# Optimization experiments

Hardware: AMD Instinct MI355X
Metric: run time of the kernel (lower is better)

Reference implementation:

```python
import jax, jax.numpy as jnp
import numpy as np

H = 4          # heads (both HGTConv and MHA)
LN_EPS = 1e-5
ALPHA = 0.1


def _ln(x, g, b):
    m = x.mean(-1, keepdims=True)
    v = ((x - m) ** 2).mean(-1, keepdims=True)
    return (x - m) * jax.lax.rsqrt(v + LN_EPS) * g + b


def _kqv(x, Wk, bk, Wq, bq, Wv, bv, D):
    N = x.shape[0]
    k = (x @ Wk.T + bk).reshape(N, H, D)
    q = (x @ Wq.T + bq).reshape(N, H, D)
    v = (x @ Wv.T + bv).reshape(N, H, D)
    return k, q, v


def _hgt_edge(q_dst, k_src, v_src, a_rel, m_rel, p_rel, src, dst, n_dst):
    """PyG HGTConv message passing for one edge type: relation-transform,
    per-dst-node softmax, weighted scatter-sum."""
    D = q_dst.shape[-1]
    k = jnp.einsum('nhd,hde->nhe', k_src, a_rel)   # [N_src,H,D]
    v = jnp.einsum('nhd,hde->nhe', v_src, m_rel)
    logit = (q_dst[dst] * k[src]).sum(-1) * p_rel / np.sqrt(D)   # [E,H]
    mx = jax.ops.segment_max(logit, dst, num_segments=n_dst)
    e = jnp.exp(logit - mx[dst])
    s = jax.ops.segment_sum(e, dst, num_segments=n_dst)
    a = e / (s[dst] + 1e-16)
    return jax.ops.segment_sum(v[src] * a[..., None], dst, num_segments=n_dst)  # [N_dst,H,D]


def _hgt_out(agg, x, Wout, bout, skip):
    N, dim = x.shape
    o = jax.nn.gelu(agg.reshape(N, dim), approximate=False) @ Wout.T + bout
    a = jax.nn.sigmoid(skip)
    return a * o + (1.0 - a) * x


def _mha(x, Wi, bi, Wo, bo):
    # self-attention over all entities as a single sequence (batch=1)
    N, dim = x.shape
    D = dim // H
    q, k, v = jnp.split(x @ Wi.T + bi, 3, axis=-1)
    q = q.reshape(N, H, D).transpose(1, 0, 2)
    k = k.reshape(N, H, D).transpose(1, 0, 2)
    v = v.reshape(N, H, D).transpose(1, 0, 2)
    att = jax.nn.softmax(jnp.einsum('hnd,hmd->hnm', q, k) / np.sqrt(D), axis=-1)
    o = jnp.einsum('hnm,hmd->hnd', att, v).transpose(1, 0, 2).reshape(N, dim)
    return o @ Wo.T + bo


def _forward(x_entity, x_passage, query_emb,
             Wk_ent, bk_ent, Wq_ent, bq_ent, Wv_ent, bv_ent, Wout_ent, bout_ent, skip_ent,
             Wk_psg, bk_psg, Wq_psg, bq_psg, Wv_psg, bv_psg, Wout_psg, bout_psg, skip_psg,
             a_e2p, m_e2p, p_e2p, a_p2e, m_p2e, p_p2e,
             mha_in_w, mha_in_b, mha_out_w, mha_out_b,
             ln_ent_g, ln_ent_b, ln_psg_g, ln_psg_b,
             w1, b1, w2, b2,
             e2p_src, e2p_dst, p2e_src, p2e_dst):
    N_e, dim = x_entity.shape
    N_p = x_passage.shape[0]
    D = dim // H
    # ---- HGTConv ----
    k_e, q_e, v_e = _kqv(x_entity, Wk_ent, bk_ent, Wq_ent, bq_ent, Wv_ent, bv_ent, D)
    k_p, q_p, v_p = _kqv(x_passage, Wk_psg, bk_psg, Wq_psg, bq_psg, Wv_psg, bv_psg, D)
    agg_p = _hgt_edge(q_p, k_e, v_e, a_e2p, m_e2p, p_e2p, e2p_src, e2p_dst, N_p)
    agg_e = _hgt_edge(q_e, k_p, v_p, a_p2e, m_p2e, p_p2e, p2e_src, p2e_dst, N_e)
    h_ent = _hgt_out(agg_e, x_entity, Wout_ent, bout_ent, skip_ent)
    h_psg = _hgt_out(agg_p, x_passage, Wout_psg, bout_psg, skip_psg)
    # ---- global entity attention + residual mix + LN ----
    h_glob = _mha(h_ent, mha_in_w, mha_in_b, mha_out_w, mha_out_b)
    h_ent = _ln((1.0 - ALPHA) * h_ent + ALPHA * h_glob, ln_ent_g, ln_ent_b)
    # ---- gather-scale-scatter entity -> passage (kernel target) ----
    q = query_emb.reshape(-1)
    rel = jax.nn.sigmoid(h_ent @ q)                          # [N_e]
    w_ent = h_ent[e2p_src] * rel[e2p_src][:, None]           # gather + scale
    ctx = jax.ops.segment_sum(w_ent, e2p_dst, num_segments=N_p)  # scatter-add
    h_psg = _ln(h_psg + ctx, ln_psg_g, ln_psg_b)
    # ---- scoring head ----
    feats = jnp.concatenate([h_psg, jnp.broadcast_to(q, (N_p, dim))], axis=-1)
    scores = (jax.nn.relu(feats @ w1.T + b1) @ w2.T + b2).squeeze(-1)
    return scores


def setup_inputs() -> dict:
    key = jax.random.key(0)
    N_E, N_P, DIM, NE = 4096, 4096, 256, 262144
    D = DIM // H
    ks = iter(jax.random.split(key, 64))
    def rn(shape, s=1.0):
        return jax.random.normal(next(ks), shape, jnp.float32) * s
    w = 0.05
    inp = {
        'x_entity': rn((N_E, DIM)),
        'x_passage': rn((N_P, DIM)),
        'query_emb': rn((DIM,)),
    }
    for t in ('ent', 'psg'):
        inp['Wk_' + t] = rn((DIM, DIM), w); inp['bk_' + t] = jnp.zeros((DIM,))
        inp['Wq_' + t] = rn((DIM, DIM), w); inp['bq_' + t] = jnp.zeros((DIM,))
        inp['Wv_' + t] = rn((DIM, DIM), w); inp['bv_' + t] = jnp.zeros((DIM,))
        inp['Wout_' + t] = rn((DIM, DIM), w); inp['bout_' + t] = jnp.zeros((DIM,))
        inp['skip_' + t] = jnp.ones(())
    for e in ('e2p', 'p2e'):
        inp['a_' + e] = rn((H, D, D), w)
        inp['m_' + e] = rn((H, D, D), w)
        inp['p_' + e] = jnp.ones((H,))
    inp['mha_in_w'] = rn((3 * DIM, DIM), w); inp['mha_in_b'] = jnp.zeros((3 * DIM,))
    inp['mha_out_w'] = rn((DIM, DIM), w); inp['mha_out_b'] = jnp.zeros((DIM,))
    inp['ln_ent_g'] = jnp.ones((DIM,)); inp['ln_ent_b'] = jnp.zeros((DIM,))
    inp['ln_psg_g'] = jnp.ones((DIM,)); inp['ln_psg_b'] = jnp.zeros((DIM,))
    inp['w1'] = rn((DIM, 2 * DIM), w); inp['b1'] = jnp.zeros((DIM,))
    inp['w2'] = rn((1, DIM), w); inp['b2'] = jnp.zeros((1,))
    inp['e2p_src'] = jax.random.randint(next(ks), (NE,), 0, N_E, jnp.int32)
    inp['e2p_dst'] = jax.random.randint(next(ks), (NE,), 0, N_P, jnp.int32)
    inp['p2e_src'] = jax.random.randint(next(ks), (NE,), 0, N_P, jnp.int32)
    inp['p2e_dst'] = jax.random.randint(next(ks), (NE,), 0, N_E, jnp.int32)
    return inp


def reference(x_entity, x_passage, query_emb,
              Wk_ent, bk_ent, Wq_ent, bq_ent, Wv_ent, bv_ent, Wout_ent, bout_ent, skip_ent,
              Wk_psg, bk_psg, Wq_psg, bq_psg, Wv_psg, bv_psg, Wout_psg, bout_psg, skip_psg,
              a_e2p, m_e2p, p_e2p, a_p2e, m_p2e, p_p2e,
              mha_in_w, mha_in_b, mha_out_w, mha_out_b,
              ln_ent_g, ln_ent_b, ln_psg_g, ln_psg_b,
              w1, b1, w2, b2,
              e2p_src, e2p_dst, p2e_src, p2e_dst):
    return _forward(x_entity, x_passage, query_emb,
                    Wk_ent, bk_ent, Wq_ent, bq_ent, Wv_ent, bv_ent, Wout_ent, bout_ent, skip_ent,
                    Wk_psg, bk_psg, Wq_psg, bq_psg, Wv_psg, bv_psg, Wout_psg, bout_psg, skip_psg,
                    a_e2p, m_e2p, p_e2p, a_p2e, m_p2e, p_p2e,
                    mha_in_w, mha_in_b, mha_out_w, mha_out_b,
                    ln_ent_g, ln_ent_b, ln_psg_g, ln_psg_b,
                    w1, b1, w2, b2,
                    e2p_src, e2p_dst, p2e_src, p2e_dst)
```

## Files before the change

### kernel.cpp

```cpp
#include <hip/hip_runtime.h>
#include <hip/hip_bf16.h>
#include <math.h>

#define DIM 256
#define NHEAD 4
#define HD 64
#define MSPLIT 4

typedef __attribute__((ext_vector_type(8))) short short8b;
typedef __attribute__((ext_vector_type(4))) float f32x4;

union B8 { uint4 u; short8b v; };

__device__ __forceinline__ float sigmoidf_(float x) { return 1.0f / (1.0f + __expf(-x)); }
__device__ __forceinline__ float geluf_(float x) {
    return 0.5f * x * (1.0f + erff(x * 0.70710678118654752440f));
}
__device__ __forceinline__ float wave_sum64(float v) {
    v += __shfl_xor(v, 32); v += __shfl_xor(v, 16); v += __shfl_xor(v, 8);
    v += __shfl_xor(v, 4);  v += __shfl_xor(v, 2);  v += __shfl_xor(v, 1);
    return v;
}
__device__ __forceinline__ unsigned short f2bf(float f) {
    union { float f; unsigned int u; } a; a.f = f;
    unsigned int u = a.u;
    unsigned int r = (u + 0x7FFFu + ((u >> 16) & 1u)) >> 16;
    return (unsigned short)r;
}
__device__ __forceinline__ unsigned int pk2bf(float lo, float hi) {
    return (unsigned int)f2bf(lo) | ((unsigned int)f2bf(hi) << 16);
}

template<int IN_GELU, int OUT_MODE, int WBF>
__launch_bounds__(256)
__global__ void gemm_kernel(const float* __restrict__ A, int lda,
                            const float* __restrict__ W0, const float* __restrict__ W1,
                            const float* __restrict__ W2, int ldw,
                            const float* __restrict__ B0, const float* __restrict__ B1,
                            const float* __restrict__ B2,
                            float* __restrict__ C, int ldc, int Kin,
                            const float* __restrict__ xres,
                            const float* __restrict__ skipv,
                            float* __restrict__ scores,
                            const float* __restrict__ w2v,
                            const float* __restrict__ b2v,
                            unsigned short* __restrict__ Cbf)
{
    __shared__ float As[16][68];
    __shared__ float Ws[16][68];
    const int t = threadIdx.x;
    const int r0 = blockIdx.y * 64;
    const int c0 = blockIdx.x * 64;
    const int widx = c0 >> 8;
    const float* W  = (widx == 0) ? W0 : (widx == 1 ? W1 : W2);
    const float* Bv = (widx == 0) ? B0 : (widx == 1 ? B1 : B2);
    const int cw = c0 & 255;

    const int lrow = t >> 2;
    const int lk   = (t & 3) << 2;
    const int ty = t >> 4, tx = t & 15;

    const float* Aptr = A + (size_t)(r0 + lrow) * lda + lk;
    const float* Wptr = W + (size_t)(cw + lrow) * ldw + lk;

    float acc[4][4] = {};
    for (int k0 = 0; k0 < Kin; k0 += 16) {
        float4 av = *reinterpret_cast<const float4*>(Aptr + k0);
        float4 wv = *reinterpret_cast<const float4*>(Wptr + k0);
        if (IN_GELU) {
            av.x = geluf_(av.x); av.y = geluf_(av.y);
            av.z = geluf_(av.z); av.w = geluf_(av.w);
        }
        As[lk + 0][lrow] = av.x; As[lk + 1][lrow] = av.y;
        As[lk + 2][lrow] = av.z; As[lk + 3][lrow] = av.w;
        Ws[lk + 0][lrow] = wv.x; Ws[lk + 1][lrow] = wv.y;
        Ws[lk + 2][lrow] = wv.z; Ws[lk + 3][lrow] = wv.w;
        __syncthreads();
#pragma unroll
        for (int k = 0; k < 16; ++k) {
            const float4 a = *reinterpret_cast<const float4*>(&As[k][ty << 2]);
            const float4 b = *reinterpret_cast<const float4*>(&Ws[k][tx << 2]);
            const float ar[4] = {a.x, a.y, a.z, a.w};
            const float br[4] = {b.x, b.y, b.z, b.w};
#pragma unroll
            for (int i = 0; i < 4; ++i)
#pragma unroll
                for (int j = 0; j < 4; ++j)
                    acc[i][j] = fmaf(ar[i], br[j], acc[i][j]);
        }
        __syncthreads();
    }

    float bias[4];
#pragma unroll
    for (int j = 0; j < 4; ++j) bias[j] = Bv[cw + (tx << 2) + j];

    if (OUT_MODE == 0) {
#pragma unroll
        for (int i = 0; i < 4; ++i) {
            const int r = r0 + (ty << 2) + i;
            float4 st;
            st.x = acc[i][0] + bias[0]; st.y = acc[i][1] + bias[1];
            st.z = acc[i][2] + bias[2]; st.w = acc[i][3] + bias[3];
            *reinterpret_cast<float4*>(&C[(size_t)r * ldc + c0 + (tx << 2)]) = st;
            if (WBF) {
                ushort4 sb;
                sb.x = f2bf(st.x); sb.y = f2bf(st.y); sb.z = f2bf(st.z); sb.w = f2bf(st.w);
                *reinterpret_cast<ushort4*>(&Cbf[(size_t)r * ldc + c0 + (tx << 2)]) = sb;
            }
        }
    } else if (OUT_MODE == 1) {
        const float sg = sigmoidf_(skipv[0]);
#pragma unroll
        for (int i = 0; i < 4; ++i) {
            const int r = r0 + (ty << 2) + i;
            const float4 xv = *reinterpret_cast<const float4*>(&xres[(size_t)r * ldc + c0 + (tx << 2)]);
            float4 st;
            st.x = sg * (acc[i][0] + bias[0]) + (1.f - sg) * xv.x;
            st.y = sg * (acc[i][1] + bias[1]) + (1.f - sg) * xv.y;
            st.z = sg * (acc[i][2] + bias[2]) + (1.f - sg) * xv.z;
            st.w = sg * (acc[i][3] + bias[3]) + (1.f - sg) * xv.w;
            *reinterpret_cast<float4*>(&C[(size_t)r * ldc + c0 + (tx << 2)]) = st;
        }
    } else {
        float wv[4];
#pragma unroll
        for (int j = 0; j < 4; ++j) wv[j] = w2v[c0 + (tx << 2) + j];
#pragma unroll
        for (int i = 0; i < 4; ++i) {
            float p = 0.f;
#pragma unroll
            for (int j = 0; j < 4; ++j)
                p = fmaf(fmaxf(acc[i][j] + bias[j], 0.f), wv[j], p);
            if (c0 == 0 && tx == 0) p += b2v[0];
            atomicAdd(&scores[r0 + (ty << 2) + i], p);
        }
    }
}

__launch_bounds__(256)
__global__ void rel_transform_kernel(const float* __restrict__ kin, int ldin,
                                     const float* __restrict__ arel,
                                     float* __restrict__ kout)
{
    __shared__ float Al[64][68];
    __shared__ float Kl[64][65];
    const int t = threadIdx.x;
    const int r0 = blockIdx.x * 64;
    const int h = blockIdx.y;
    const float* ah = arel + h * 4096;
    for (int i = t; i < 1024; i += 256) {
        const int rr = i >> 4, c4 = (i & 15) << 2;
        const float4 av = *reinterpret_cast<const float4*>(&ah[rr * 64 + c4]);
        *reinterpret_cast<float4*>(&Al[rr][c4]) = av;
        const float4 kv = *reinterpret_cast<const float4*>(&kin[(size_t)(r0 + rr) * ldin + h * 64 + c4]);
        Kl[rr][c4 + 0] = kv.x; Kl[rr][c4 + 1] = kv.y;
        Kl[rr][c4 + 2] = kv.z; Kl[rr][c4 + 3] = kv.w;
    }
    __syncthreads();
    const int r  = t & 63;
    const int e0 = (t >> 6) << 4;
    float acc[16] = {};
    for (int d = 0; d < 64; ++d) {
        const float kv = Kl[r][d];
#pragma unroll
        for (int u4 = 0; u4 < 4; ++u4) {
            const float4 a = *reinterpret_cast<const float4*>(&Al[d][e0 + (u4 << 2)]);
            acc[u4 * 4 + 0] = fmaf(kv, a.x, acc[u4 * 4 + 0]);
            acc[u4 * 4 + 1] = fmaf(kv, a.y, acc[u4 * 4 + 1]);
            acc[u4 * 4 + 2] = fmaf(kv, a.z, acc[u4 * 4 + 2]);
            acc[u4 * 4 + 3] = fmaf(kv, a.w, acc[u4 * 4 + 3]);
        }
    }
#pragma unroll
    for (int u4 = 0; u4 < 4; ++u4) {
        float4 st = {acc[u4 * 4 + 0], acc[u4 * 4 + 1], acc[u4 * 4 + 2], acc[u4 * 4 + 3]};
        *reinterpret_cast<float4*>(&kout[(size_t)(r0 + r) * 256 + h * 64 + e0 + (u4 << 2)]) = st;
    }
}

__global__ void edge_count_kernel(const int* __restrict__ dst, int* __restrict__ cnt, int E)
{
    const int i = blockIdx.x * 256 + threadIdx.x;
    if (i < E) atomicAdd(&cnt[dst[i]], 1);
}

__launch_bounds__(1024)
__global__ void scan_kernel(const int* __restrict__ cnt, int* __restrict__ indptr,
                            int* __restrict__ cursor)
{
    __shared__ int sh[1024];
    const int t = threadIdx.x;
    const int4 v = *reinterpret_cast<const int4*>(&cnt[t << 2]);
    const int sum = v.x + v.y + v.z + v.w;
    sh[t] = sum;
    __syncthreads();
    for (int off = 1; off < 1024; off <<= 1) {
        int x = 0;
        if (t >= off) x = sh[t - off];
        __syncthreads();
        if (t >= off) sh[t] += x;
        __syncthreads();
    }
    int run = sh[t] - sum;
    const int base = t << 2;
    if (t == 0) indptr[0] = 0;
    cursor[base + 0] = run; run += v.x; indptr[base + 1] = run;
    cursor[base + 1] = run; run += v.y; indptr[base + 2] = run;
    cursor[base + 2] = run; run += v.z; indptr[base + 3] = run;
    cursor[base + 3] = run; run += v.w; indptr[base + 4] = run;
}

__global__ void edge_scatter_kernel(const int* __restrict__ src, const int* __restrict__ dst,
                                    int* __restrict__ cursor, int* __restrict__ ssrc, int E)
{
    const int i = blockIdx.x * 256 + threadIdx.x;
    if (i < E) {
        const int p = atomicAdd(&cursor[dst[i]], 1);
        ssrc[p] = src[i];
    }
}

__launch_bounds__(256)
__global__ void hgt_attn_kernel(const float* __restrict__ qdst,
                                const float* __restrict__ kt,
                                const float* __restrict__ vt,
                                const float* __restrict__ prel,
                                const int* __restrict__ indptr,
                                const int* __restrict__ ssrc,
                                float* __restrict__ agg)
{
    const int n = blockIdx.x * 4 + (threadIdx.x >> 6);
    const int lane = threadIdx.x & 63;
    const int h = lane >> 4;
    const int d4 = (lane & 15) << 2;
    const float4 q = *reinterpret_cast<const float4*>(&qdst[(size_t)n * 768 + h * 64 + d4]);
    const float ps = prel[h] * 0.125f;
    const int e0 = indptr[n], e1 = indptr[n + 1];
    float m = -1e30f, s = 0.f;
    float4 acc = {0.f, 0.f, 0.f, 0.f};
    for (int e = e0; e < e1; ++e) {
        const int sr = ssrc[e];
        const float4 k = *reinterpret_cast<const float4*>(&kt[(size_t)sr * 256 + h * 64 + d4]);
        float d = q.x * k.x + q.y * k.y + q.z * k.z + q.w * k.w;
        d += __shfl_xor(d, 1); d += __shfl_xor(d, 2);
        d += __shfl_xor(d, 4); d += __shfl_xor(d, 8);
        const float logit = d * ps;
        const float mn = fmaxf(m, logit);
        const float f = __expf(m - mn);
        const float p = __expf(logit - mn);
        s = s * f + p;
        const float4 v = *reinterpret_cast<const float4*>(&vt[(size_t)sr * 256 + h * 64 + d4]);
        acc.x = acc.x * f + p * v.x;
        acc.y = acc.y * f + p * v.y;
        acc.z = acc.z * f + p * v.z;
        acc.w = acc.w * f + p * v.w;
        m = mn;
    }
    const float inv = 1.f / (s + 1e-16f);
    float4 st = {acc.x * inv, acc.y * inv, acc.z * inv, acc.w * inv};
    *reinterpret_cast<float4*>(&agg[(size_t)n * 256 + h * 64 + d4]) = st;
}

__launch_bounds__(256)
__global__ void vtrans_kernel(const unsigned short* __restrict__ qkv_bf,
                              unsigned short* __restrict__ vt, int N)
{
    __shared__ unsigned short tile[64][66];
    const int t = threadIdx.x;
    const int k0 = blockIdx.x * 64;
    const int h = blockIdx.y;
    {
        const int key = t >> 2;
        const int d0 = (t & 3) << 4;
        const unsigned short* src = qkv_bf + (size_t)(k0 + key) * 768 + 512 + h * 64 + d0;
        const uint4 a = *reinterpret_cast<const uint4*>(src);
        const uint4 b = *reinterpret_cast<const uint4*>(src + 8);
        const unsigned int w_[8] = {a.x, a.y, a.z, a.w, b.x, b.y, b.z, b.w};
#pragma unroll
        for (int j = 0; j < 8; ++j) {
            tile[d0 + 2 * j][key]     = (unsigned short)(w_[j] & 0xffff);
            tile[d0 + 2 * j + 1][key] = (unsigned short)(w_[j] >> 16);
        }
    }
    __syncthreads();
    {
        const int d = t >> 2;
        const int kk = (t & 3) << 4;
        unsigned int o_[8];
#pragma unroll
        for (int j = 0; j < 8; ++j)
            o_[j] = (unsigned int)tile[d][kk + 2 * j] | ((unsigned int)tile[d][kk + 2 * j + 1] << 16);
        unsigned short* dstp = vt + (size_t)(h * 64 + d) * N + k0 + kk;
        uint4 s0 = {o_[0], o_[1], o_[2], o_[3]};
        uint4 s1 = {o_[4], o_[5], o_[6], o_[7]};
        *reinterpret_cast<uint4*>(dstp) = s0;
        *reinterpret_cast<uint4*>(dstp + 8) = s1;
    }
}

__launch_bounds__(256)
__global__ void mha_mfma_kernel(const unsigned short* __restrict__ qkv_bf,
                                const unsigned short* __restrict__ vt_bf,
                                float* __restrict__ opart,
                                float* __restrict__ mpart,
                                float* __restrict__ lpart,
                                int N)
{
    const int lane = threadIdx.x & 63;
    const int g = lane >> 4;
    const int q15 = lane & 15;
    const int gw = blockIdx.x * 4 + (threadIdx.x >> 6);
    const int split = gw & (MSPLIT - 1);
    const int gq = gw >> 2;
    const int h = gq >> 8;
    const int qt = gq & 255;
    const int q0 = qt * 16;
    const int kbeg = split * (N / MSPLIT);
    const int kend = kbeg + (N / MSPLIT);

    B8 qf0, qf1;
    {
        const unsigned short* qp = qkv_bf + (size_t)(q0 + q15) * 768 + h * 64 + g * 8;
        qf0.u = *reinterpret_cast<const uint4*>(qp);
        qf1.u = *reinterpret_cast<const uint4*>(qp + 32);
    }

    f32x4 o0 = {0,0,0,0}, o1 = {0,0,0,0}, o2 = {0,0,0,0}, o3 = {0,0,0,0};
    float m_run = -1e30f, l_run = 0.f;

    const unsigned short* kbase = qkv_bf + 256 + h * 64 + g * 8;
    const unsigned short* vbase = vt_bf + (size_t)(h * 64 + q15) * N + g * 8;
    const int sl0 = (((2 * g) & 3) << 4) + q15;
    const int sl1 = (((2 * g + 1) & 3) << 4) + q15;

    for (int ck = kbeg; ck < kend; ck += 32) {
        B8 k00, k01, k10, k11;
        const unsigned short* kp0 = kbase + (size_t)(ck + q15) * 768;
        const unsigned short* kp1 = kbase + (size_t)(ck + 16 + q15) * 768;
        k00.u = *reinterpret_cast<const uint4*>(kp0);
        k01.u = *reinterpret_cast<const uint4*>(kp0 + 32);
        k10.u = *reinterpret_cast<const uint4*>(kp1);
        k11.u = *reinterpret_cast<const uint4*>(kp1 + 32);
        f32x4 s0 = {0,0,0,0}, s1 = {0,0,0,0};
        s0 = __builtin_amdgcn_mfma_f32_16x16x32_bf16(k00.v, qf0.v, s0, 0, 0, 0);
        s0 = __builtin_amdgcn_mfma_f32_16x16x32_bf16(k01.v, qf1.v, s0, 0, 0, 0);
        s1 = __builtin_amdgcn_mfma_f32_16x16x32_bf16(k10.v, qf0.v, s1, 0, 0, 0);
        s1 = __builtin_amdgcn_mfma_f32_16x16x32_bf16(k11.v, qf1.v, s1, 0, 0, 0);

        float p[8];
        p[0] = s0.x * 0.125f; p[1] = s0.y * 0.125f; p[2] = s0.z * 0.125f; p[3] = s0.w * 0.125f;
        p[4] = s1.x * 0.125f; p[5] = s1.y * 0.125f; p[6] = s1.z * 0.125f; p[7] = s1.w * 0.125f;

        float mx = fmaxf(fmaxf(fmaxf(p[0], p[1]), fmaxf(p[2], p[3])),
                         fmaxf(fmaxf(p[4], p[5]), fmaxf(p[6], p[7])));
        mx = fmaxf(mx, __shfl_xor(mx, 16));
        mx = fmaxf(mx, __shfl_xor(mx, 32));
        const float mnew = fmaxf(m_run, mx);
        const float f = __expf(m_run - mnew);
        float sum = 0.f;
#pragma unroll
        for (int i = 0; i < 8; ++i) { p[i] = __expf(p[i] - mnew); sum += p[i]; }
        sum += __shfl_xor(sum, 16);
        sum += __shfl_xor(sum, 32);
        l_run = l_run * f + sum;
        m_run = mnew;
        o0 *= f; o1 *= f; o2 *= f; o3 *= f;

        const unsigned int c01a = pk2bf(p[0], p[1]), c23a = pk2bf(p[2], p[3]);
        const unsigned int c01b = pk2bf(p[4], p[5]), c23b = pk2bf(p[6], p[7]);
        uint4 pu;
        {
            unsigned int x0, x1;
            x0 = (unsigned int)__shfl((int)c01a, sl0); x1 = (unsigned int)__shfl((int)c01b, sl0);
            pu.x = (g < 2) ? x0 : x1;
            x0 = (unsigned int)__shfl((int)c23a, sl0); x1 = (unsigned int)__shfl((int)c23b, sl0);
            pu.y = (g < 2) ? x0 : x1;
            x0 = (unsigned int)__shfl((int)c01a, sl1); x1 = (unsigned int)__shfl((int)c01b, sl1);
            pu.z = (g < 2) ? x0 : x1;
            x0 = (unsigned int)__shfl((int)c23a, sl1); x1 = (unsigned int)__shfl((int)c23b, sl1);
            pu.w = (g < 2) ? x0 : x1;
        }
        B8 pb; pb.u = pu;

        const unsigned short* vp = vbase + ck;
        B8 vf;
        vf.u = *reinterpret_cast<const uint4*>(vp);
        o0 = __builtin_amdgcn_mfma_f32_16x16x32_bf16(vf.v, pb.v, o0, 0, 0, 0);
        vf.u = *reinterpret_cast<const uint4*>(vp + (size_t)16 * N);
        o1 = __builtin_amdgcn_mfma_f32_16x16x32_bf16(vf.v, pb.v, o1, 0, 0, 0);
        vf.u = *reinterpret_cast<const uint4*>(vp + (size_t)32 * N);
        o2 = __builtin_amdgcn_mfma_f32_16x16x32_bf16(vf.v, pb.v, o2, 0, 0, 0);
        vf.u = *reinterpret_cast<const uint4*>(vp + (size_t)48 * N);
        o3 = __builtin_amdgcn_mfma_f32_16x16x32_bf16(vf.v, pb.v, o3, 0, 0, 0);
    }

    float* op = opart + (size_t)split * N * 256 + (size_t)(q0 + q15) * 256 + h * 64 + 4 * g;
#pragma unroll
    for (int r = 0; r < 4; ++r) {
        op[0 * 16 + r] = o0[r];
        op[1 * 16 + r] = o1[r];
        op[2 * 16 + r] = o2[r];
        op[3 * 16 + r] = o3[r];
    }
    if (g == 0) {
        mpart[(size_t)(split * NHEAD + h) * N + q0 + q15] = m_run;
        lpart[(size_t)(split * NHEAD + h) * N + q0 + q15] = l_run;
    }
}

__launch_bounds__(256)
__global__ void mha_combine_kernel(const float* __restrict__ opart,
                                   const float* __restrict__ mpart,
                                   const float* __restrict__ lpart,
                                   float* __restrict__ outp, int N)
{
    const int q = blockIdx.x;
    const int c = threadIdx.x;
    const int h = c >> 6;
    const size_t base = (size_t)q * 256 + c;
    float m[MSPLIT], l[MSPLIT];
    float M = -1e30f;
#pragma unroll
    for (int s = 0; s < MSPLIT; ++s) {
        m[s] = mpart[(size_t)(s * NHEAD + h) * N + q];
        l[s] = lpart[(size_t)(s * NHEAD + h) * N + q];
        M = fmaxf(M, m[s]);
    }
    float L = 0.f, o = 0.f;
#pragma unroll
    for (int s = 0; s < MSPLIT; ++s) {
        const float w = __expf(m[s] - M);
        L += w * l[s];
        o = fmaf(w, opart[(size_t)s * N * 256 + base], o);
    }
    outp[base] = o / L;
}

__launch_bounds__(256)
__global__ void mix_ln_rel_kernel(float* __restrict__ he, const float* __restrict__ hg,
                                  const float* __restrict__ g, const float* __restrict__ b,
                                  const float* __restrict__ q, float* __restrict__ rel)
{
    const int row = (blockIdx.x * 256 + threadIdx.x) >> 6;
    const int lane = threadIdx.x & 63;
    const float4 a = *reinterpret_cast<const float4*>(&he[(size_t)row * 256 + (lane << 2)]);
    const float4 c = *reinterpret_cast<const float4*>(&hg[(size_t)row * 256 + (lane << 2)]);
    float4 v;
    v.x = 0.9f * a.x + 0.1f * c.x; v.y = 0.9f * a.y + 0.1f * c.y;
    v.z = 0.9f * a.z + 0.1f * c.z; v.w = 0.9f * a.w + 0.1f * c.w;
    const float mean = wave_sum64(v.x + v.y + v.z + v.w) * (1.f / 256.f);
    float4 d = {v.x - mean, v.y - mean, v.z - mean, v.w - mean};
    const float var = wave_sum64(d.x * d.x + d.y * d.y + d.z * d.z + d.w * d.w) * (1.f / 256.f);
    const float rs = rsqrtf(var + 1e-5f);
    const float4 gg = *reinterpret_cast<const float4*>(&g[lane << 2]);
    const float4 bb = *reinterpret_cast<const float4*>(&b[lane << 2]);
    float4 y = {d.x * rs * gg.x + bb.x, d.y * rs * gg.y + bb.y,
                d.z * rs * gg.z + bb.z, d.w * rs * gg.w + bb.w};
    *reinterpret_cast<float4*>(&he[(size_t)row * 256 + (lane << 2)]) = y;
    const float4 qq = *reinterpret_cast<const float4*>(&q[lane << 2]);
    const float dq = wave_sum64(y.x * qq.x + y.y * qq.y + y.z * qq.z + y.w * qq.w);
    if (lane == 0) rel[row] = sigmoidf_(dq);
}

__launch_bounds__(256)
__global__ void ctx_gather_kernel(const float* __restrict__ he, const float* __restrict__ rel,
                                  const int* __restrict__ indptr, const int* __restrict__ ssrc,
                                  float* __restrict__ ctx)
{
    const int gw = (blockIdx.x * 256 + threadIdx.x) >> 6;
    const int lane = threadIdx.x & 63;
    const int p = gw >> 2, qt = gw & 3;
    const int e0 = indptr[p], e1 = indptr[p + 1];
    float acc = 0.f;
    for (int e = e0; e < e1; ++e) {
        const int sr = ssrc[e];
        acc = fmaf(he[(size_t)sr * 256 + qt * 64 + lane], rel[sr], acc);
    }
    ctx[(size_t)p * 256 + qt * 64 + lane] = acc;
}

__launch_bounds__(256)
__global__ void psg_ln_kernel(float* __restrict__ hp, const float* __restrict__ ctx,
                              const float* __restrict__ g, const float* __restrict__ b)
{
    const int row = (blockIdx.x * 256 + threadIdx.x) >> 6;
    const int lane = threadIdx.x & 63;
    const float4 a = *reinterpret_cast<const float4*>(&hp[(size_t)row * 256 + (lane << 2)]);
    const float4 c = *reinterpret_cast<const float4*>(&ctx[(size_t)row * 256 + (lane << 2)]);
    float4 v = {a.x + c.x, a.y + c.y, a.z + c.z, a.w + c.w};
    const float mean = wave_sum64(v.x + v.y + v.z + v.w) * (1.f / 256.f);
    float4 d = {v.x - mean, v.y - mean, v.z - mean, v.w - mean};
    const float var = wave_sum64(d.x * d.x + d.y * d.y + d.z * d.z + d.w * d.w) * (1.f / 256.f);
    const float rs = rsqrtf(var + 1e-5f);
    const float4 gg = *reinterpret_cast<const float4*>(&g[lane << 2]);
    const float4 bb = *reinterpret_cast<const float4*>(&b[lane << 2]);
    float4 y = {d.x * rs * gg.x + bb.x, d.y * rs * gg.y + bb.y,
                d.z * rs * gg.z + bb.z, d.w * rs * gg.w + bb.w};
    *reinterpret_cast<float4*>(&hp[(size_t)row * 256 + (lane << 2)]) = y;
}

__global__ void qterm_kernel(const float* __restrict__ w1, const float* __restrict__ b1,
                             const float* __restrict__ q, float* __restrict__ qterm)
{
    __shared__ float qs[256];
    const int t = threadIdx.x;
    qs[t] = q[t];
    __syncthreads();
    float s = b1[t];
    for (int k = 0; k < 256; ++k) s = fmaf(w1[(size_t)t * 512 + 256 + k], qs[k], s);
    qterm[t] = s;
}

extern "C" void kernel_launch(void* const* d_in, const int* in_sizes, int n_in,
                              void* d_out, int out_size, void* d_ws, size_t ws_size,
                              hipStream_t stream)
{
    const float* x_ent = (const float*)d_in[0];
    const float* x_psg = (const float*)d_in[1];
    const float* q_emb = (const float*)d_in[2];
    const float* Wk_e = (const float*)d_in[3];  const float* bk_e = (const float*)d_in[4];
    const float* Wq_e = (const float*)d_in[5];  const float* bq_e = (const float*)d_in[6];
    const float* Wv_e = (const float*)d_in[7];  const float* bv_e = (const float*)d_in[8];
    const float* Wo_e = (const float*)d_in[9];  const float* bo_e = (const float*)d_in[10];
    const float* sk_e = (const float*)d_in[11];
    const float* Wk_p = (const float*)d_in[12]; const float* bk_p = (const float*)d_in[13];
    const float* Wq_p = (const float*)d_in[14]; const float* bq_p = (const float*)d_in[15];
    const float* Wv_p = (const float*)d_in[16]; const float* bv_p = (const float*)d_in[17];
    const float* Wo_p = (const float*)d_in[18]; const float* bo_p = (const float*)d_in[19];
    const float* sk_p = (const float*)d_in[20];
    const float* a_e2p = (const float*)d_in[21];
    const float* m_e2p = (const float*)d_in[22];
    const float* p_e2p = (const float*)d_in[23];
    const float* a_p2e = (const float*)d_in[24];
    const float* m_p2e = (const float*)d_in[25];
    const float* p_p2e = (const float*)d_in[26];
    const float* Wmi = (const float*)d_in[27];  const float* bmi = (const float*)d_in[28];
    const float* Wmo = (const float*)d_in[29];  const float* bmo = (const float*)d_in[30];
    const float* lng_e = (const float*)d_in[31]; const float* lnb_e = (const float*)d_in[32];
    const float* lng_p = (const float*)d_in[33]; const float* lnb_p = (const float*)d_in[34];
    const float* w1 = (const float*)d_in[35];   const float* b1 = (const float*)d_in[36];
    const float* w2 = (const float*)d_in[37];   const float* b2 = (const float*)d_in[38];
    const int* e2p_src = (const int*)d_in[39];
    const int* e2p_dst = (const int*)d_in[40];
    const int* p2e_src = (const int*)d_in[41];
    const int* p2e_dst = (const int*)d_in[42];

    const int NE = in_sizes[0] / DIM;
    const int NP = in_sizes[1] / DIM;
    const int E  = in_sizes[39];
    float* scores = (float*)d_out;

    char* wp = (char*)d_ws;
    auto alloc = [&](size_t bytes) -> void* {
        void* r = (void*)wp;
        wp += (bytes + 255) & ~(size_t)255;
        return r;
    };
    float* kqv_e = (float*)alloc((size_t)NE * 768 * 4);
    float* kqv_p = (float*)alloc((size_t)NP * 768 * 4);
    float* kt_e  = (float*)alloc((size_t)NE * 256 * 4);
    float* vt_e  = (float*)alloc((size_t)NE * 256 * 4);
    float* kt_p  = (float*)alloc((size_t)NP * 256 * 4);
    float* vt_p  = (float*)alloc((size_t)NP * 256 * 4);
    float* agg_p = (float*)alloc((size_t)NP * 256 * 4);
    float* agg_e = (float*)alloc((size_t)NE * 256 * 4);
    float* h_ent = (float*)alloc((size_t)NE * 256 * 4);
    float* h_psg = (float*)alloc((size_t)NP * 256 * 4);
    float* qkv_m = (float*)alloc((size_t)NE * 768 * 4);
    float* att_o = (float*)alloc((size_t)NE * 256 * 4);
    float* h_glob= (float*)alloc((size_t)NE * 256 * 4);
    float* relv  = (float*)alloc((size_t)NE * 4);
    float* ctxb  = (float*)alloc((size_t)NP * 256 * 4);
    float* qterm = (float*)alloc(256 * 4);
    unsigned short* qkv_bf = (unsigned short*)alloc((size_t)NE * 768 * 2);
    unsigned short* vt_bf  = (unsigned short*)alloc((size_t)256 * NE * 2);
    float* mpart = (float*)alloc((size_t)MSPLIT * NHEAD * NE * 4);
    float* lpart = (float*)alloc((size_t)MSPLIT * NHEAD * NE * 4);
    float* opart = kqv_e;
    int* cnt_a = (int*)alloc((size_t)NP * 4);
    int* cur_a = (int*)alloc((size_t)NP * 4);
    int* ip_a  = (int*)alloc((size_t)(NP + 1) * 4);
    int* ss_a  = (int*)alloc((size_t)E * 4);
    int* cnt_b = (int*)alloc((size_t)NE * 4);
    int* cur_b = (int*)alloc((size_t)NE * 4);
    int* ip_b  = (int*)alloc((size_t)(NE + 1) * 4);
    int* ss_b  = (int*)alloc((size_t)E * 4);

    hipMemsetAsync(cnt_a, 0, (size_t)NP * 4, stream);
    hipMemsetAsync(cnt_b, 0, (size_t)NE * 4, stream);
    hipMemsetAsync(d_out, 0, (size_t)out_size * 4, stream);

    const int eb = (E + 255) / 256;
    edge_count_kernel<<<eb, 256, 0, stream>>>(e2p_dst, cnt_a, E);
    edge_count_kernel<<<eb, 256, 0, stream>>>(p2e_dst, cnt_b, E);
    scan_kernel<<<1, 1024, 0, stream>>>(cnt_a, ip_a, cur_a);
    scan_kernel<<<1, 1024, 0, stream>>>(cnt_b, ip_b, cur_b);
    edge_scatter_kernel<<<eb, 256, 0, stream>>>(e2p_src, e2p_dst, cur_a, ss_a, E);
    edge_scatter_kernel<<<eb, 256, 0, stream>>>(p2e_src, p2e_dst, cur_b, ss_b, E);

    gemm_kernel<0,0,0><<<dim3(12, NE / 64), 256, 0, stream>>>(
        x_ent, 256, Wk_e, Wq_e, Wv_e, 256, bk_e, bq_e, bv_e,
        kqv_e, 768, 256, nullptr, nullptr, nullptr, nullptr, nullptr, nullptr);
    gemm_kernel<0,0,0><<<dim3(12, NP / 64), 256, 0, stream>>>(
        x_psg, 256, Wk_p, Wq_p, Wv_p, 256, bk_p, bq_p, bv_p,
        kqv_p, 768, 256, nullptr, nullptr, nullptr, nullptr, nullptr, nullptr);

    rel_transform_kernel<<<dim3(NE / 64, NHEAD), 256, 0, stream>>>(kqv_e + 0,   768, a_e2p, kt_e);
    rel_transform_kernel<<<dim3(NE / 64, NHEAD), 256, 0, stream>>>(kqv_e + 512, 768, m_e2p, vt_e);
    rel_transform_kernel<<<dim3(NP / 64, NHEAD), 256, 0, stream>>>(kqv_p + 0,   768, a_p2e, kt_p);
    rel_transform_kernel<<<dim3(NP / 64, NHEAD), 256, 0, stream>>>(kqv_p + 512, 768, m_p2e, vt_p);

    hgt_attn_kernel<<<NP / 4, 256, 0, stream>>>(kqv_p + 256, kt_e, vt_e, p_e2p, ip_a, ss_a, agg_p);
    hgt_attn_kernel<<<NE / 4, 256, 0, stream>>>(kqv_e + 256, kt_p, vt_p, p_p2e, ip_b, ss_b, agg_e);

    gemm_kernel<1,1,0><<<dim3(4, NE / 64), 256, 0, stream>>>(
        agg_e, 256, Wo_e, Wo_e, Wo_e, 256, bo_e, bo_e, bo_e,
        h_ent, 256, 256, x_ent, sk_e, nullptr, nullptr, nullptr, nullptr);
    gemm_kernel<1,1,0><<<dim3(4, NP / 64), 256, 0, stream>>>(
        agg_p, 256, Wo_p, Wo_p, Wo_p, 256, bo_p, bo_p, bo_p,
        h_psg, 256, 256, x_psg, sk_p, nullptr, nullptr, nullptr, nullptr);

    gemm_kernel<0,0,1><<<dim3(12, NE / 64), 256, 0, stream>>>(
        h_ent, 256, Wmi, Wmi + 65536, Wmi + 131072, 256, bmi, bmi + 256, bmi + 512,
        qkv_m, 768, 256, nullptr, nullptr, nullptr, nullptr, nullptr, qkv_bf);
    vtrans_kernel<<<dim3(NE / 64, NHEAD), 256, 0, stream>>>(qkv_bf, vt_bf, NE);
    mha_mfma_kernel<<<NHEAD * (NE / 16) * MSPLIT / 4, 256, 0, stream>>>(
        qkv_bf, vt_bf, opart, mpart, lpart, NE);
    mha_combine_kernel<<<NE, 256, 0, stream>>>(opart, mpart, lpart, att_o, NE);
    gemm_kernel<0,0,0><<<dim3(4, NE / 64), 256, 0, stream>>>(
        att_o, 256, Wmo, Wmo, Wmo, 256, bmo, bmo, bmo,
        h_glob, 256, 256, nullptr, nullptr, nullptr, nullptr, nullptr, nullptr);

    mix_ln_rel_kernel<<<NE / 4, 256, 0, stream>>>(h_ent, h_glob, lng_e, lnb_e, q_emb, relv);

    ctx_gather_kernel<<<NP, 256, 0, stream>>>(h_ent, relv, ip_a, ss_a, ctxb);
    psg_ln_kernel<<<NP / 4, 256, 0, stream>>>(h_psg, ctxb, lng_p, lnb_p);

    qterm_kernel<<<1, 256, 0, stream>>>(w1, b1, q_emb, qterm);
    gemm_kernel<0,2,0><<<dim3(4, NP / 64), 256, 0, stream>>>(
        h_psg, 256, w1, w1, w1, 512, qterm, qterm, qterm,
        nullptr, 256, 256, nullptr, nullptr, scores, w2, b2, nullptr);
}
```

Baseline: 758.6 us.

## Move dense projection GEMMs to bf16 MFMA with pre-converted weights and activations

Adds kernels that convert the twelve 256x256 weight matrices and the input or GELU'd activations to bf16. It then replaces the fp32 FMA tiled GEMMs for the KQV, output, MHA-in and MHA-out projections with a bf16 MFMA kernel that reads operands straight from global memory. The MHA combine now writes bf16 so the out-projection can read it directly, and the MHA-in GEMM writes only bf16. This moves the GEMMs onto the matrix cores at the cost of extra conversion launches, reduced precision, uncoalesced scalar epilogue stores and no LDS reuse.

```diff
diff --git a/kernel.cpp b/kernel.cpp
--- a/kernel.cpp
+++ b/kernel.cpp
@@ -31,7 +31,121 @@
     return (unsigned int)f2bf(lo) | ((unsigned int)f2bf(hi) << 16);
 }
 
-template<int IN_GELU, int OUT_MODE, int WBF>
+template<int DO_GELU>
+__launch_bounds__(256)
+__global__ void cvt_bf16_kernel(const float* __restrict__ src,
+                                unsigned short* __restrict__ dst, int n8)
+{
+    const int i = blockIdx.x * 256 + threadIdx.x;
+    if (i >= n8) return;
+    float4 a = reinterpret_cast<const float4*>(src)[2 * i];
+    float4 b = reinterpret_cast<const float4*>(src)[2 * i + 1];
+    if (DO_GELU) {
+        a.x = geluf_(a.x); a.y = geluf_(a.y); a.z = geluf_(a.z); a.w = geluf_(a.w);
+        b.x = geluf_(b.x); b.y = geluf_(b.y); b.z = geluf_(b.z); b.w = geluf_(b.w);
+    }
+    ushort4 lo = {f2bf(a.x), f2bf(a.y), f2bf(a.z), f2bf(a.w)};
+    ushort4 hi = {f2bf(b.x), f2bf(b.y), f2bf(b.z), f2bf(b.w)};
+    reinterpret_cast<ushort4*>(dst)[2 * i] = lo;
+    reinterpret_cast<ushort4*>(dst)[2 * i + 1] = hi;
+}
+
+__launch_bounds__(256)
+__global__ void cvt_w_kernel(const float* __restrict__ W0, const float* __restrict__ W1,
+                             const float* __restrict__ W2, const float* __restrict__ W3,
+                             const float* __restrict__ W4, const float* __restrict__ W5,
+                             const float* __restrict__ W6, const float* __restrict__ W7,
+                             const float* __restrict__ W8, const float* __restrict__ W9,
+                             const float* __restrict__ W10, const float* __restrict__ W11,
+                             unsigned short* __restrict__ arena)
+{
+    const float* s;
+    switch (blockIdx.y) {
+        case 0: s = W0; break;  case 1: s = W1; break;  case 2: s = W2; break;
+        case 3: s = W3; break;  case 4: s = W4; break;  case 5: s = W5; break;
+        case 6: s = W6; break;  case 7: s = W7; break;  case 8: s = W8; break;
+        case 9: s = W9; break;  case 10: s = W10; break; default: s = W11; break;
+    }
+    const int i = blockIdx.x * 256 + threadIdx.x;
+    unsigned short* dst = arena + (size_t)blockIdx.y * 65536;
+    float4 a = reinterpret_cast<const float4*>(s)[2 * i];
+    float4 b = reinterpret_cast<const float4*>(s)[2 * i + 1];
+    ushort4 lo = {f2bf(a.x), f2bf(a.y), f2bf(a.z), f2bf(a.w)};
+    ushort4 hi = {f2bf(b.x), f2bf(b.y), f2bf(b.z), f2bf(b.w)};
+    reinterpret_cast<ushort4*>(dst)[2 * i] = lo;
+    reinterpret_cast<ushort4*>(dst)[2 * i + 1] = hi;
+}
+
+template<int OUT_MODE, int WF32, int WBF>
+__launch_bounds__(256)
+__global__ void bgemm_kernel(const unsigned short* __restrict__ Abf,
+                             const unsigned short* __restrict__ W0b,
+                             const unsigned short* __restrict__ W1b,
+                             const unsigned short* __restrict__ W2b,
+                             const float* __restrict__ B0, const float* __restrict__ B1,
+                             const float* __restrict__ B2,
+                             float* __restrict__ C, int ldc,
+                             unsigned short* __restrict__ Cbf, int ldcb,
+                             const float* __restrict__ xres,
+                             const float* __restrict__ skipv)
+{
+    const int t = threadIdx.x;
+    const int lane = t & 63;
+    const int wid = t >> 6;
+    const int col16 = lane & 15;
+    const int oct = lane >> 4;
+    const int r0 = blockIdx.y * 64 + wid * 16;
+    const int c0 = blockIdx.x * 64;
+    const int widx = c0 >> 8;
+    const unsigned short* W = (widx == 0) ? W0b : (widx == 1 ? W1b : W2b);
+    const float* Bv = (widx == 0) ? B0 : (widx == 1 ? B1 : B2);
+    const int cw = c0 & 255;
+
+    const unsigned short* aptr = Abf + (size_t)(r0 + col16) * 256 + oct * 8;
+    const unsigned short* wptr = W + (size_t)(cw + col16) * 256 + oct * 8;
+
+    f32x4 acc0 = {0,0,0,0}, acc1 = {0,0,0,0}, acc2 = {0,0,0,0}, acc3 = {0,0,0,0};
+#pragma unroll
+    for (int k0 = 0; k0 < 256; k0 += 32) {
+        B8 af, w0, w1, w2, w3;
+        af.u = *reinterpret_cast<const uint4*>(aptr + k0);
+        w0.u = *reinterpret_cast<const uint4*>(wptr + k0);
+        w1.u = *reinterpret_cast<const uint4*>(wptr + k0 + 16 * 256);
+        w2.u = *reinterpret_cast<const uint4*>(wptr + k0 + 32 * 256);
+        w3.u = *reinterpret_cast<const uint4*>(wptr + k0 + 48 * 256);
+        acc0 = __builtin_amdgcn_mfma_f32_16x16x32_bf16(af.v, w0.v, acc0, 0, 0, 0);
+        acc1 = __builtin_amdgcn_mfma_f32_16x16x32_bf16(af.v, w1.v, acc1, 0, 0, 0);
+        acc2 = __builtin_amdgcn_mfma_f32_16x16x32_bf16(af.v, w2.v, acc2, 0, 0, 0);
+        acc3 = __builtin_amdgcn_mfma_f32_16x16x32_bf16(af.v, w3.v, acc3, 0, 0, 0);
+    }
+
+    float bias[4];
+#pragma unroll
+    for (int j = 0; j < 4; ++j) bias[j] = Bv[cw + j * 16 + col16];
+    float sg = 0.f;
+    if (OUT_MODE == 1) sg = sigmoidf_(skipv[0]);
+
+    const float av[4][4] = {
+        {acc0.x, acc0.y, acc0.z, acc0.w}, {acc1.x, acc1.y, acc1.z, acc1.w},
+        {acc2.x, acc2.y, acc2.z, acc2.w}, {acc3.x, acc3.y, acc3.z, acc3.w}};
+#pragma unroll
+    for (int r = 0; r < 4; ++r) {
+        const int row = r0 + oct * 4 + r;
+#pragma unroll
+        for (int j = 0; j < 4; ++j) {
+            const int col = c0 + j * 16 + col16;
+            float v = av[j][r] + bias[j];
+            if (OUT_MODE == 1) {
+                const float xv = xres[(size_t)row * ldc + col];
+                v = sg * v + (1.f - sg) * xv;
+            }
+            if (WF32) C[(size_t)row * ldc + col] = v;
+            if (WBF)  Cbf[(size_t)row * ldcb + col] = f2bf(v);
+        }
+    }
+}
+
+template<int IN_GELU, int OUT_MODE>
 __launch_bounds__(256)
 __global__ void gemm_kernel(const float* __restrict__ A, int lda,
                             const float* __restrict__ W0, const float* __restrict__ W1,
@@ -39,12 +153,9 @@
                             const float* __restrict__ B0, const float* __restrict__ B1,
                             const float* __restrict__ B2,
                             float* __restrict__ C, int ldc, int Kin,
-                            const float* __restrict__ xres,
-                            const float* __restrict__ skipv,
                             float* __restrict__ scores,
                             const float* __restrict__ w2v,
-                            const float* __restrict__ b2v,
-                            unsigned short* __restrict__ Cbf)
+                            const float* __restrict__ b2v)
 {
     __shared__ float As[16][68];
     __shared__ float Ws[16][68];
@@ -98,29 +209,10 @@
     if (OUT_MODE == 0) {
 #pragma unroll
         for (int i = 0; i < 4; ++i) {
-            const int r = r0 + (ty << 2) + i;
             float4 st;
             st.x = acc[i][0] + bias[0]; st.y = acc[i][1] + bias[1];
             st.z = acc[i][2] + bias[2]; st.w = acc[i][3] + bias[3];
-            *reinterpret_cast<float4*>(&C[(size_t)r * ldc + c0 + (tx << 2)]) = st;
-            if (WBF) {
-                ushort4 sb;
-                sb.x = f2bf(st.x); sb.y = f2bf(st.y); sb.z = f2bf(st.z); sb.w = f2bf(st.w);
-                *reinterpret_cast<ushort4*>(&Cbf[(size_t)r * ldc + c0 + (tx << 2)]) = sb;
-            }
-        }
-    } else if (OUT_MODE == 1) {
-        const float sg = sigmoidf_(skipv[0]);
-#pragma unroll
-        for (int i = 0; i < 4; ++i) {
-            const int r = r0 + (ty << 2) + i;
-            const float4 xv = *reinterpret_cast<const float4*>(&xres[(size_t)r * ldc + c0 + (tx << 2)]);
-            float4 st;
-            st.x = sg * (acc[i][0] + bias[0]) + (1.f - sg) * xv.x;
-            st.y = sg * (acc[i][1] + bias[1]) + (1.f - sg) * xv.y;
-            st.z = sg * (acc[i][2] + bias[2]) + (1.f - sg) * xv.z;
-            st.w = sg * (acc[i][3] + bias[3]) + (1.f - sg) * xv.w;
-            *reinterpret_cast<float4*>(&C[(size_t)r * ldc + c0 + (tx << 2)]) = st;
+            *reinterpret_cast<float4*>(&C[(size_t)(r0 + (ty << 2) + i) * ldc + c0 + (tx << 2)]) = st;
         }
     } else {
         float wv[4];
@@ -413,7 +505,7 @@
 __global__ void mha_combine_kernel(const float* __restrict__ opart,
                                    const float* __restrict__ mpart,
                                    const float* __restrict__ lpart,
-                                   float* __restrict__ outp, int N)
+                                   unsigned short* __restrict__ outpb, int N)
 {
     const int q = blockIdx.x;
     const int c = threadIdx.x;
@@ -434,7 +526,7 @@
         L += w * l[s];
         o = fmaf(w, opart[(size_t)s * N * 256 + base], o);
     }
-    outp[base] = o / L;
+    outpb[base] = f2bf(o / L);
 }
 
 __launch_bounds__(256)
@@ -567,14 +659,19 @@
     float* agg_e = (float*)alloc((size_t)NE * 256 * 4);
     float* h_ent = (float*)alloc((size_t)NE * 256 * 4);
     float* h_psg = (float*)alloc((size_t)NP * 256 * 4);
-    float* qkv_m = (float*)alloc((size_t)NE * 768 * 4);
-    float* att_o = (float*)alloc((size_t)NE * 256 * 4);
     float* h_glob= (float*)alloc((size_t)NE * 256 * 4);
     float* relv  = (float*)alloc((size_t)NE * 4);
     float* ctxb  = (float*)alloc((size_t)NP * 256 * 4);
     float* qterm = (float*)alloc(256 * 4);
-    unsigned short* qkv_bf = (unsigned short*)alloc((size_t)NE * 768 * 2);
-    unsigned short* vt_bf  = (unsigned short*)alloc((size_t)256 * NE * 2);
+    unsigned short* warena  = (unsigned short*)alloc((size_t)12 * 65536 * 2);
+    unsigned short* xe_bf   = (unsigned short*)alloc((size_t)NE * 256 * 2);
+    unsigned short* xp_bf   = (unsigned short*)alloc((size_t)NP * 256 * 2);
+    unsigned short* ge_bf   = (unsigned short*)alloc((size_t)NE * 256 * 2);
+    unsigned short* gp_bf   = (unsigned short*)alloc((size_t)NP * 256 * 2);
+    unsigned short* hent_bf = (unsigned short*)alloc((size_t)NE * 256 * 2);
+    unsigned short* atto_bf = (unsigned short*)alloc((size_t)NE * 256 * 2);
+    unsigned short* qkv_bf  = (unsigned short*)alloc((size_t)NE * 768 * 2);
+    unsigned short* vt_bf   = (unsigned short*)alloc((size_t)256 * NE * 2);
     float* mpart = (float*)alloc((size_t)MSPLIT * NHEAD * NE * 4);
     float* lpart = (float*)alloc((size_t)MSPLIT * NHEAD * NE * 4);
     float* opart = kqv_e;
@@ -591,6 +688,12 @@
     hipMemsetAsync(cnt_b, 0, (size_t)NE * 4, stream);
     hipMemsetAsync(d_out, 0, (size_t)out_size * 4, stream);
 
+    cvt_w_kernel<<<dim3(32, 12), 256, 0, stream>>>(
+        Wk_e, Wq_e, Wv_e, Wo_e, Wk_p, Wq_p, Wv_p, Wo_p,
+        Wmi, Wmi + 65536, Wmi + 131072, Wmo, warena);
+    cvt_bf16_kernel<0><<<NE * 256 / 2048, 256, 0, stream>>>(x_ent, xe_bf, NE * 32);
+    cvt_bf16_kernel<0><<<NP * 256 / 2048, 256, 0, stream>>>(x_psg, xp_bf, NP * 32);
+
     const int eb = (E + 255) / 256;
     edge_count_kernel<<<eb, 256, 0, stream>>>(e2p_dst, cnt_a, E);
     edge_count_kernel<<<eb, 256, 0, stream>>>(p2e_dst, cnt_b, E);
@@ -599,12 +702,12 @@
     edge_scatter_kernel<<<eb, 256, 0, stream>>>(e2p_src, e2p_dst, cur_a, ss_a, E);
     edge_scatter_kernel<<<eb, 256, 0, stream>>>(p2e_src, p2e_dst, cur_b, ss_b, E);
 
-    gemm_kernel<0,0,0><<<dim3(12, NE / 64), 256, 0, stream>>>(
-        x_ent, 256, Wk_e, Wq_e, Wv_e, 256, bk_e, bq_e, bv_e,
-        kqv_e, 768, 256, nullptr, nullptr, nullptr, nullptr, nullptr, nullptr);
-    gemm_kernel<0,0,0><<<dim3(12, NP / 64), 256, 0, stream>>>(
-        x_psg, 256, Wk_p, Wq_p, Wv_p, 256, bk_p, bq_p, bv_p,
-        kqv_p, 768, 256, nullptr, nullptr, nullptr, nullptr, nullptr, nullptr);
+    bgemm_kernel<0,1,0><<<dim3(12, NE / 64), 256, 0, stream>>>(
+        xe_bf, warena, warena + 65536, warena + 131072, bk_e, bq_e, bv_e,
+        kqv_e, 768, nullptr, 0, nullptr, nullptr);
+    bgemm_kernel<0,1,0><<<dim3(12, NP / 64), 256, 0, stream>>>(
+        xp_bf, warena + 4*65536, warena + 5*65536, warena + 6*65536, bk_p, bq_p, bv_p,
+        kqv_p, 768, nullptr, 0, nullptr, nullptr);
 
     rel_transform_kernel<<<dim3(NE / 64, NHEAD), 256, 0, stream>>>(kqv_e + 0,   768, a_e2p, kt_e);
     rel_transform_kernel<<<dim3(NE / 64, NHEAD), 256, 0, stream>>>(kqv_e + 512, 768, m_e2p, vt_e);
@@ -614,23 +717,26 @@
     hgt_attn_kernel<<<NP / 4, 256, 0, stream>>>(kqv_p + 256, kt_e, vt_e, p_e2p, ip_a, ss_a, agg_p);
     hgt_attn_kernel<<<NE / 4, 256, 0, stream>>>(kqv_e + 256, kt_p, vt_p, p_p2e, ip_b, ss_b, agg_e);
 
-    gemm_kernel<1,1,0><<<dim3(4, NE / 64), 256, 0, stream>>>(
-        agg_e, 256, Wo_e, Wo_e, Wo_e, 256, bo_e, bo_e, bo_e,
-        h_ent, 256, 256, x_ent, sk_e, nullptr, nullptr, nullptr, nullptr);
-    gemm_kernel<1,1,0><<<dim3(4, NP / 64), 256, 0, stream>>>(
-        agg_p, 256, Wo_p, Wo_p, Wo_p, 256, bo_p, bo_p, bo_p,
-        h_psg, 256, 256, x_psg, sk_p, nullptr, nullptr, nullptr, nullptr);
-
-    gemm_kernel<0,0,1><<<dim3(12, NE / 64), 256, 0, stream>>>(
-        h_ent, 256, Wmi, Wmi + 65536, Wmi + 131072, 256, bmi, bmi + 256, bmi + 512,
-        qkv_m, 768, 256, nullptr, nullptr, nullptr, nullptr, nullptr, qkv_bf);
+    cvt_bf16_kernel<1><<<NE * 256 / 2048, 256, 0, stream>>>(agg_e, ge_bf, NE * 32);
+    cvt_bf16_kernel<1><<<NP * 256 / 2048, 256, 0, stream>>>(agg_p, gp_bf, NP * 32);
+    bgemm_kernel<1,1,1><<<dim3(4, NE / 64), 256, 0, stream>>>(
+        ge_bf, warena + 3*65536, warena + 3*65536, warena + 3*65536, bo_e, bo_e, bo_e,
+        h_ent, 256, hent_bf, 256, x_ent, sk_e);
+    bgemm_kernel<1,1,0><<<dim3(4, NP / 64), 256, 0, stream>>>(
+        gp_bf, warena + 7*65536, warena + 7*65536, warena + 7*65536, bo_p, bo_p, bo_p,
+        h_psg, 256, nullptr, 0, x_psg, sk_p);
+
+    bgemm_kernel<0,0,1><<<dim3(12, NE / 64), 256, 0, stream>>>(
+        hent_bf, warena + 8*65536, warena + 9*65536, warena + 10*65536,
+        bmi, bmi + 256, bmi + 512,
+        nullptr, 0, qkv_bf, 768, nullptr, nullptr);
     vtrans_kernel<<<dim3(NE / 64, NHEAD), 256, 0, stream>>>(qkv_bf, vt_bf, NE);
     mha_mfma_kernel<<<NHEAD * (NE / 16) * MSPLIT / 4, 256, 0, stream>>>(
         qkv_bf, vt_bf, opart, mpart, lpart, NE);
-    mha_combine_kernel<<<NE, 256, 0, stream>>>(opart, mpart, lpart, att_o, NE);
-    gemm_kernel<0,0,0><<<dim3(4, NE / 64), 256, 0, stream>>>(
-        att_o, 256, Wmo, Wmo, Wmo, 256, bmo, bmo, bmo,
-        h_glob, 256, 256, nullptr, nullptr, nullptr, nullptr, nullptr, nullptr);
+    mha_combine_kernel<<<NE, 256, 0, stream>>>(opart, mpart, lpart, atto_bf, NE);
+    bgemm_kernel<0,1,0><<<dim3(4, NE / 64), 256, 0, stream>>>(
+        atto_bf, warena + 11*65536, warena + 11*65536, warena + 11*65536, bmo, bmo, bmo,
+        h_glob, 256, nullptr, 0, nullptr, nullptr);
 
     mix_ln_rel_kernel<<<NE / 4, 256, 0, stream>>>(h_ent, h_glob, lng_e, lnb_e, q_emb, relv);
 
@@ -638,7 +744,7 @@
     psg_ln_kernel<<<NP / 4, 256, 0, stream>>>(h_psg, ctxb, lng_p, lnb_p);
 
     qterm_kernel<<<1, 256, 0, stream>>>(w1, b1, q_emb, qterm);
-    gemm_kernel<0,2,0><<<dim3(4, NP / 64), 256, 0, stream>>>(
+    gemm_kernel<0,2><<<dim3(4, NP / 64), 256, 0, stream>>>(
         h_psg, 256, w1, w1, w1, 512, qterm, qterm, qterm,
-        nullptr, 256, 256, nullptr, nullptr, scores, w2, b2, nullptr);
-}
+        nullptr, 256, 256, scores, w2, b2);
+}
```

Measured after the change: 717.2 us. 5.5% less time.
